# Optimization experiments

Measured on AMD Instinct MI355X. Metric: run time of the kernel, lower is better.

The kernel has to match this reference:

```python
import jax, jax.numpy as jnp
import numpy as np

N = 100_000          # nodes
E_RAND = 1_600_000   # random edges (avg degree 16)
IN, H, F, SEQ = 64, 4, 16, 10
FLAT = H * F * SEQ   # 640, MLP input width
MLP_DIMS = [FLAT, 180, 150, 128, 80, 64, 32, 1]


def setup_inputs() -> dict:
    key = jax.random.key(0)
    ks = jax.random.split(key, 32)
    x = jax.random.normal(ks[0], (N, IN), jnp.float32)
    # edges + self loops (dgl.add_self_loop)
    src = jnp.concatenate([jax.random.randint(ks[1], (E_RAND,), 0, N), jnp.arange(N)]).astype(jnp.int32)
    dst = jnp.concatenate([jax.random.randint(ks[2], (E_RAND,), 0, N), jnp.arange(N)]).astype(jnp.int32)
    inp = {"x": x, "src": src, "dst": dst}
    # GATConv params (fc has no bias in DGL; bias added post-aggregation)
    inp["fc_w"] = (jax.random.normal(ks[3], (IN, H * F), jnp.float32) / np.sqrt(IN).astype(np.float32))
    inp["bias"] = jnp.zeros((H * F,), jnp.float32)
    inp["attn_l"] = jax.random.normal(ks[4], (H, F), jnp.float32) * 0.1
    inp["attn_r"] = jax.random.normal(ks[5], (H, F), jnp.float32) * 0.1
    # deep MLP params
    for i in range(7):
        di, do = MLP_DIMS[i], MLP_DIMS[i + 1]
        inp[f"w{i+1}"] = jax.random.normal(ks[6 + i], (di, do), jnp.float32) / np.sqrt(di).astype(np.float32)
        inp[f"b{i+1}"] = jnp.zeros((do,), jnp.float32)
    inp["wt"] = jax.random.normal(ks[20], (FLAT, 1), jnp.float32) / np.sqrt(FLAT).astype(np.float32)
    return inp


def reference(x, src, dst, fc_w, bias, attn_l, attn_r,
              w1, b1, w2, b2, w3, b3, w4, b4, w5, b5, w6, b6, w7, b7, wt):
    # --- GATConv ---
    feat = (x @ fc_w).reshape(N, H, F)                      # [N,H,F]
    el = jnp.einsum('nhf,hf->nh', feat, attn_l)             # [N,H]
    er = jnp.einsum('nhf,hf->nh', feat, attn_r)
    e = jax.nn.leaky_relu(el[src] + er[dst], 0.2)           # [E,H]
    # edge softmax over incoming edges of each dst node
    m = jax.ops.segment_max(e, dst, num_segments=N)         # [N,H]
    ez = jnp.exp(e - m[dst])
    denom = jax.ops.segment_sum(ez, dst, num_segments=N)
    alpha = ez / denom[dst]                                 # [E,H]
    msg = alpha[:, :, None] * feat[src]                     # [E,H,F]
    out = jax.ops.segment_sum(msg, dst, num_segments=N) + bias.reshape(1, H, F)
    # --- flatten SEQ nodes per path, deep MLP + linear_trans ---
    g = out.reshape(N // SEQ, FLAT)                         # [P,640]
    h = g
    layers = [(w1, b1), (w2, b2), (w3, b3), (w4, b4), (w5, b5), (w6, b6), (w7, b7)]
    for i, (w, b) in enumerate(layers):
        h = h @ w + b
        if i < len(layers) - 1:
            h = jax.nn.relu(h)
    wx = g @ wt                                             # [P,1]
    return h + wx
```

## Files before the change

### kernel.cpp

```cpp
#include <hip/hip_runtime.h>
#include <hip/hip_bf16.h>
#include <hip/hip_fp16.h>

#define N_NODES 100000
#define P_PATHS 10000
#define NBUK 391
#define FEAT_BLKS 391
#define HIST_BLKS 416
#define WPREP_BLKS 94

typedef __attribute__((ext_vector_type(8))) short s16x8;
typedef __attribute__((ext_vector_type(4))) short s16x4;
typedef __attribute__((ext_vector_type(4))) float f32x4;
typedef __attribute__((ext_vector_type(8))) _Float16 f16x8;

__device__ __forceinline__ short f2bf(float v) {
    return __builtin_bit_cast(short, __float2bfloat16(v));
}
__device__ __forceinline__ float bf2f(short s) {
    return __bfloat162float(__builtin_bit_cast(__hip_bfloat16, s));
}
__device__ __forceinline__ float h2f(short s) {
    return __half2float(__builtin_bit_cast(__half, s));
}
__device__ __forceinline__ short f2h(float v) {
    return __builtin_bit_cast(short, __float2half(v));
}

__global__ __launch_bounds__(256) void k_fused1(const float* __restrict__ x,
                                                const float* __restrict__ fc_w,
                                                const float* __restrict__ attn_l,
                                                const float* __restrict__ attn_r,
                                                __half* __restrict__ feat,
                                                float* __restrict__ el,
                                                float* __restrict__ er,
                                                const int* __restrict__ dst,
                                                int* __restrict__ buktot,
                                                const float* __restrict__ w1,
                                                const float* __restrict__ w2,
                                                const float* __restrict__ w3,
                                                const float* __restrict__ w4,
                                                const float* __restrict__ w5,
                                                const float* __restrict__ w6,
                                                short* __restrict__ wf, int E) {
    __shared__ float s_w[64 * 64];
    __shared__ float s_wx[64 * 16];
    __shared__ int hcnt[NBUK];
    int tid = threadIdx.x;
    int bb = blockIdx.x;

    if (bb < FEAT_BLKS) {
        for (int i = tid; i < 4096; i += 256) s_w[i] = fc_w[i];
        __syncthreads();
        for (int i = tid; i < 1024; i += 256) {
            int k = i >> 4, c = i & 15;
            float v = 0.f;
            if (c < 8) {
                int h = c & 3;
                const float* av = (c < 4) ? attn_l : attn_r;
                for (int f = 0; f < 16; ++f) v += s_w[k * 64 + h * 16 + f] * av[h * 16 + f];
            }
            s_wx[i] = v;
        }
        __syncthreads();

        int w = tid >> 6, l = tid & 63;
        int c_lane = l & 15, kg = l >> 4;

        s16x8 wh[5][2], wlo[5][2];
#pragma unroll
        for (int ct = 0; ct < 5; ++ct)
#pragma unroll
            for (int ks = 0; ks < 2; ++ks) {
                s16x8 h8, l8;
#pragma unroll
                for (int i = 0; i < 8; ++i) {
                    int k = ks * 32 + kg * 8 + i;
                    float v = (ct < 4) ? s_w[k * 64 + ct * 16 + c_lane]
                                       : s_wx[k * 16 + c_lane];
                    short hi = f2bf(v);
                    h8[i] = hi;
                    l8[i] = f2bf(v - bf2f(hi));
                }
                wh[ct][ks] = h8;
                wlo[ct][ks] = l8;
            }

        int nbase = bb * 256 + w * 64;
#pragma unroll 1
        for (int mt = 0; mt < 4; ++mt) {
            int m0 = nbase + mt * 16;
            if (m0 >= N_NODES) break;
            int arow = m0 + c_lane;
            size_t axoff = (size_t)(arow < N_NODES ? arow : N_NODES - 1) * 64;
            s16x8 ah[2], alo[2];
#pragma unroll
            for (int ks = 0; ks < 2; ++ks) {
                const float* xp = x + axoff + ks * 32 + kg * 8;
                float4 v0 = *(const float4*)xp;
                float4 v1 = *(const float4*)(xp + 4);
                float vv[8] = {v0.x, v0.y, v0.z, v0.w, v1.x, v1.y, v1.z, v1.w};
                s16x8 h8, l8;
#pragma unroll
                for (int i = 0; i < 8; ++i) {
                    short hi = f2bf(vv[i]);
                    h8[i] = hi;
                    l8[i] = f2bf(vv[i] - bf2f(hi));
                }
                ah[ks] = h8;
                alo[ks] = l8;
            }
            int r0 = m0 + kg * 4;
#pragma unroll
            for (int ct = 0; ct < 5; ++ct) {
                f32x4 acc = {0.f, 0.f, 0.f, 0.f};
#pragma unroll
                for (int ks = 0; ks < 2; ++ks) {
                    acc = __builtin_amdgcn_mfma_f32_16x16x32_bf16(ah[ks], wh[ct][ks], acc, 0, 0, 0);
                    acc = __builtin_amdgcn_mfma_f32_16x16x32_bf16(ah[ks], wlo[ct][ks], acc, 0, 0, 0);
                    acc = __builtin_amdgcn_mfma_f32_16x16x32_bf16(alo[ks], wh[ct][ks], acc, 0, 0, 0);
                }
                if (ct < 4) {
#pragma unroll
                    for (int j = 0; j < 4; ++j) {
                        int r = r0 + j;
                        if (r < N_NODES)
                            feat[(size_t)r * 64 + ct * 16 + c_lane] = __float2half(acc[j]);
                    }
                } else {
                    if (c_lane < 4) {
#pragma unroll
                        for (int j = 0; j < 4; ++j) {
                            int r = r0 + j;
                            if (r < N_NODES) el[r * 4 + c_lane] = acc[j];
                        }
                    } else if (c_lane < 8) {
#pragma unroll
                        for (int j = 0; j < 4; ++j) {
                            int r = r0 + j;
                            if (r < N_NODES) er[r * 4 + (c_lane - 4)] = acc[j];
                        }
                    }
                }
            }
        }
    } else if (bb < FEAT_BLKS + HIST_BLKS) {
        int hb = bb - FEAT_BLKS;
        for (int i = tid; i < NBUK; i += 256) hcnt[i] = 0;
        __syncthreads();
#pragma unroll
        for (int j = 0; j < 4; ++j) {
            int i = hb * 4096 + j * 1024 + tid * 4;
            if (i + 3 < E) {
                int4 d4 = *(const int4*)(dst + i);
                atomicAdd(&hcnt[d4.x >> 8], 1);
                atomicAdd(&hcnt[d4.y >> 8], 1);
                atomicAdd(&hcnt[d4.z >> 8], 1);
                atomicAdd(&hcnt[d4.w >> 8], 1);
            } else {
                for (int k = i; k < E && k < i + 4; ++k)
                    atomicAdd(&hcnt[dst[k] >> 8], 1);
            }
        }
        __syncthreads();
        for (int i = tid; i < NBUK; i += 256)
            if (hcnt[i]) atomicAdd(buktot + i, hcnt[i]);
    } else {
        const int nblk[6] = {240, 60, 40, 20, 12, 4};
        const int din_[6] = {640, 180, 150, 128, 80, 64};
        const int dout_[6] = {180, 150, 128, 80, 64, 32};
        const int ks_[6]  = {20, 6, 5, 4, 3, 2};
        const int off_[6] = {0, 122880, 153600, 174080, 184320, 190464};
        const float* wp[6] = {w1, w2, w3, w4, w5, w6};

        int b = (bb - FEAT_BLKS - HIST_BLKS) * 4 + (tid >> 6);
        int layer = 0;
        while (layer < 5 && b >= nblk[layer]) { b -= nblk[layer]; ++layer; }
        int KS = ks_[layer];
        int ct = b / KS, ks = b % KS;
        int l = tid & 63;
        int c = ct * 16 + (l & 15);
        int k0 = ks * 32 + ((l >> 4) * 8);
        int din = din_[layer], dout = dout_[layer];
        const float* w = wp[layer];
        s16x8 vh;
#pragma unroll
        for (int i = 0; i < 8; ++i) {
            int k = k0 + i;
            float v = (k < din && c < dout) ? w[k * dout + c] : 0.f;
            vh[i] = f2h(v);
        }
        size_t o = (size_t)off_[layer] + ((size_t)(ct * KS + ks) * 64 + l) * 8;
        *(s16x8*)(wf + o) = vh;
    }
}

__global__ __launch_bounds__(512) void k_scanB(const int* __restrict__ buktot,
                                               int* __restrict__ bukstart,
                                               int* __restrict__ bukptr,
                                               int* __restrict__ rowptr, int E) {
    __shared__ int s[512];
    int tid = threadIdx.x;
    int v = (tid < NBUK) ? buktot[tid] : 0;
    s[tid] = v;
    __syncthreads();
    for (int off = 1; off < 512; off <<= 1) {
        int t = (tid >= off) ? s[tid - off] : 0;
        __syncthreads();
        s[tid] += t;
        __syncthreads();
    }
    int excl = s[tid] - v;
    if (tid < NBUK) { bukstart[tid] = excl; bukptr[tid] = excl; }
    if (tid == 0) { bukstart[NBUK] = E; rowptr[N_NODES] = E; }
}

__global__ __launch_bounds__(256) void k_bucketA(const int* __restrict__ src,
                                                 const int* __restrict__ dst,
                                                 int* __restrict__ bukptr,
                                                 unsigned* __restrict__ pair, int E) {
    __shared__ int cnt[NBUK];
    __shared__ int base[NBUK];
    int tid = threadIdx.x;
    for (int i = tid; i < NBUK; i += 256) cnt[i] = 0;
    __syncthreads();
    int b0 = blockIdx.x * 2048;
    int s[8], d[8], off[8];
#pragma unroll
    for (int j = 0; j < 8; ++j) {
        int i = b0 + j * 256 + tid;
        if (i < E) {
            s[j] = src[i];
            d[j] = dst[i];
            off[j] = atomicAdd(&cnt[d[j] >> 8], 1);
        } else {
            d[j] = -1; s[j] = 0; off[j] = 0;
        }
    }
    __syncthreads();
    for (int i = tid; i < NBUK; i += 256)
        base[i] = cnt[i] ? atomicAdd(bukptr + i, cnt[i]) : 0;
    __syncthreads();
#pragma unroll
    for (int j = 0; j < 8; ++j) {
        if (d[j] >= 0) {
            int pos = base[d[j] >> 8] + off[j];
            pair[pos] = (unsigned)s[j] | ((unsigned)(d[j] & 255) << 17);
        }
    }
}

__global__ __launch_bounds__(256) void k_bucketC(const unsigned* __restrict__ pair,
                                                 const int* __restrict__ bukstart,
                                                 int* __restrict__ rowptr,
                                                 int* __restrict__ csr, int E) {
    __shared__ int cnt[256];
    __shared__ int s[256];
    __shared__ int wofs[256];
    int buk = blockIdx.x, tid = threadIdx.x;
    int p0 = bukstart[buk], p1 = bukstart[buk + 1];
    cnt[tid] = 0;
    __syncthreads();
    for (int i = p0 + tid; i < p1; i += 256)
        atomicAdd(&cnt[pair[i] >> 17], 1);
    __syncthreads();
    int v = cnt[tid];
    s[tid] = v;
    __syncthreads();
    for (int off = 1; off < 256; off <<= 1) {
        int t = (tid >= off) ? s[tid - off] : 0;
        __syncthreads();
        s[tid] += t;
        __syncthreads();
    }
    int r = p0 + s[tid] - v;
    wofs[tid] = r;
    int node = (buk << 8) + tid;
    if (node < N_NODES) rowptr[node] = r;
    __syncthreads();
    for (int i = p0 + tid; i < p1; i += 256) {
        unsigned p = pair[i];
        int pos = atomicAdd(&wofs[p >> 17], 1);
        csr[pos] = (int)(p & 0x1FFFFu);
    }
}

__global__ __launch_bounds__(256) void k_agg(const int* __restrict__ rowptr,
                                             const int* __restrict__ csr,
                                             const float* __restrict__ el,
                                             const float* __restrict__ er,
                                             const __half* __restrict__ feat,
                                             const float* __restrict__ bias,
                                             __half* __restrict__ agg) {
    int tid = threadIdx.x;
    int wave = tid >> 6, lane = tid & 63;
    int slot = lane >> 4;
    int fl = lane & 15;
    int n = blockIdx.x * 4 + wave;
    if (n >= N_NODES) return;
    int h = fl >> 2;
    float ern = er[(size_t)n * 4 + h];
    int e0 = rowptr[n], e1 = rowptr[n + 1];
    f32x4 a0 = {0.f, 0.f, 0.f, 0.f}, a1 = {0.f, 0.f, 0.f, 0.f};
    float den0 = 0.f, den1 = 0.f;
    int e = e0 + slot;
    for (; e + 4 < e1; e += 8) {
        int s0 = csr[e], s1 = csr[e + 4];
        s16x4 v0 = *(const s16x4*)(feat + (size_t)s0 * 64 + fl * 4);
        s16x4 v1 = *(const s16x4*)(feat + (size_t)s1 * 64 + fl * 4);
        float ev0 = el[(size_t)s0 * 4 + h] + ern;
        float ev1 = el[(size_t)s1 * 4 + h] + ern;
        ev0 = ev0 > 0.f ? ev0 : 0.2f * ev0;
        ev1 = ev1 > 0.f ? ev1 : 0.2f * ev1;
        float ez0 = __expf(ev0);
        float ez1 = __expf(ev1);
#pragma unroll
        for (int t = 0; t < 4; ++t) {
            a0[t] += ez0 * h2f(v0[t]);
            a1[t] += ez1 * h2f(v1[t]);
        }
        den0 += ez0;
        den1 += ez1;
    }
    for (; e < e1; e += 4) {
        int s0 = csr[e];
        s16x4 v0 = *(const s16x4*)(feat + (size_t)s0 * 64 + fl * 4);
        float ev0 = el[(size_t)s0 * 4 + h] + ern;
        ev0 = ev0 > 0.f ? ev0 : 0.2f * ev0;
        float ez0 = __expf(ev0);
#pragma unroll
        for (int t = 0; t < 4; ++t)
            a0[t] += ez0 * h2f(v0[t]);
        den0 += ez0;
    }
    f32x4 a;
    float den = den0 + den1;
#pragma unroll
    for (int t = 0; t < 4; ++t) a[t] = a0[t] + a1[t];
#pragma unroll
    for (int t = 0; t < 4; ++t) {
        a[t] += __shfl_xor(a[t], 32);
        a[t] += __shfl_xor(a[t], 16);
    }
    den += __shfl_xor(den, 32);
    den += __shfl_xor(den, 16);
    if (slot == 0) {
        float inv = 1.f / den;
        s16x4 o;
        o[0] = f2h(a[0] * inv + bias[fl * 4 + 0]);
        o[1] = f2h(a[1] * inv + bias[fl * 4 + 1]);
        o[2] = f2h(a[2] * inv + bias[fl * 4 + 2]);
        o[3] = f2h(a[3] * inv + bias[fl * 4 + 3]);
        *(s16x4*)(agg + (size_t)n * 64 + fl * 4) = o;
    }
}

template <int KS, int CT>
__device__ __forceinline__ void mfma_layer16(const short* sa, int sstride,
                                             short* dst_,
                                             const short* __restrict__ wf,
                                             const float* __restrict__ bias,
                                             int dout, int w, int l) {
    int abase = (l & 15) * sstride + ((l >> 4) * 8);
    int c_lane = l & 15;
    for (int ct = w; ct < CT; ct += 4) {
        f32x4 acc = {0.f, 0.f, 0.f, 0.f};
        const f16x8* wp = (const f16x8*)wf + (size_t)(ct * KS) * 64 + l;
#pragma unroll
        for (int ks = 0; ks < KS; ++ks) {
            f16x8 av = *(const f16x8*)(sa + abase + ks * 32);
            f16x8 wv = wp[ks * 64];
            acc = __builtin_amdgcn_mfma_f32_16x16x32_f16(av, wv, acc, 0, 0, 0);
        }
        int c = ct * 16 + c_lane;
        float bb = (c < dout) ? bias[c] : 0.f;
        int row0 = (l >> 4) * 4;
#pragma unroll
        for (int j = 0; j < 4; ++j) {
            float v = acc[j] + bb;
            v = v > 0.f ? v : 0.f;
            dst_[(row0 + j) * 200 + c] = f2h(v);
        }
    }
}

__global__ __launch_bounds__(256) void k_mlp(const __half* __restrict__ agg,
                                             const short* __restrict__ wf,
                                             const float* __restrict__ b1,
                                             const float* __restrict__ b2,
                                             const float* __restrict__ b3,
                                             const float* __restrict__ b4,
                                             const float* __restrict__ b5,
                                             const float* __restrict__ b6,
                                             const float* __restrict__ w7,
                                             const float* __restrict__ b7,
                                             const float* __restrict__ wt,
                                             float* __restrict__ outp) {
    __shared__ __align__(16) short smem[13600];
    __shared__ float wx[16];
    short* g  = smem;
    short* h0 = smem + 10368;
    short* h1 = smem;

    int tid = threadIdx.x;
    int w = tid >> 6, l = tid & 63;
    int p0 = blockIdx.x * 16;

    const s16x8* a8 = (const s16x8*)(agg + (size_t)p0 * 640);
    for (int i = tid; i < 16 * 80; i += 256) {
        int r = i / 80, c8 = (i % 80) * 8;
        *(s16x8*)(g + r * 648 + c8) = a8[i];
    }

    if (tid < 128) {
        int path = tid >> 3, sub = tid & 7;
        const __half* gr = agg + (size_t)(p0 + path) * 640;
        float acc = 0.f;
        for (int k = sub * 4; k < 640; k += 32) {
            s16x4 gv = *(const s16x4*)(gr + k);
            float4 wv = *(const float4*)(wt + k);
            acc += h2f(gv[0]) * wv.x + h2f(gv[1]) * wv.y
                 + h2f(gv[2]) * wv.z + h2f(gv[3]) * wv.w;
        }
        acc += __shfl_xor(acc, 1);
        acc += __shfl_xor(acc, 2);
        acc += __shfl_xor(acc, 4);
        if (sub == 0) wx[path] = acc;
    }
    __syncthreads();

    mfma_layer16<20, 12>(g, 648, h0, wf + 0,      b1, 180, w, l);
    __syncthreads();
    mfma_layer16<6, 10>(h0, 200, h1, wf + 122880, b2, 150, w, l);
    __syncthreads();
    mfma_layer16<5, 8>(h1, 200, h0, wf + 153600, b3, 128, w, l);
    __syncthreads();
    mfma_layer16<4, 5>(h0, 200, h1, wf + 174080, b4, 80, w, l);
    {
        int r = tid >> 4, c = 80 + (tid & 15);
        h1[r * 200 + c] = 0;
    }
    __syncthreads();
    mfma_layer16<3, 4>(h1, 200, h0, wf + 184320, b5, 64, w, l);
    __syncthreads();
    mfma_layer16<2, 2>(h0, 200, h1, wf + 190464, b6, 32, w, l);
    __syncthreads();

    if (tid < 16) {
        float acc = b7[0];
#pragma unroll
        for (int k = 0; k < 32; ++k)
            acc += h2f(h1[tid * 200 + k]) * w7[k];
        outp[p0 + tid] = acc + wx[tid];
    }
}

extern "C" void kernel_launch(void* const* d_in, const int* in_sizes, int n_in,
                              void* d_out, int out_size, void* d_ws, size_t ws_size,
                              hipStream_t stream) {
    const float* x      = (const float*)d_in[0];
    const int*   src    = (const int*)d_in[1];
    const int*   dst    = (const int*)d_in[2];
    const float* fc_w   = (const float*)d_in[3];
    const float* bias   = (const float*)d_in[4];
    const float* attn_l = (const float*)d_in[5];
    const float* attn_r = (const float*)d_in[6];
    const float* w1 = (const float*)d_in[7];  const float* b1 = (const float*)d_in[8];
    const float* w2 = (const float*)d_in[9];  const float* b2 = (const float*)d_in[10];
    const float* w3 = (const float*)d_in[11]; const float* b3 = (const float*)d_in[12];
    const float* w4 = (const float*)d_in[13]; const float* b4 = (const float*)d_in[14];
    const float* w5 = (const float*)d_in[15]; const float* b5 = (const float*)d_in[16];
    const float* w6 = (const float*)d_in[17]; const float* b6 = (const float*)d_in[18];
    const float* w7 = (const float*)d_in[19]; const float* b7 = (const float*)d_in[20];
    const float* wt = (const float*)d_in[21];
    int E = in_sizes[1];

    float* ws      = (float*)d_ws;
    __half* feat   = (__half*)ws;
    float* el      = ws + 6400000;
    float* er      = ws + 6800000;
    __half* agg    = (__half*)(ws + 7200000);
    unsigned* pair = (unsigned*)(ws + 10400000);
    int*   rowptr  = (int*)(ws + 13600000);
    int*   buktot  = (int*)(ws + 13700004);
    int*   bukstart= (int*)(ws + 13700400);
    int*   bukptr  = (int*)(ws + 13700800);
    int*   csr     = (int*)(ws + 13701200);
    short* wf      = (short*)(ws + 13701200 + E);

    int nwgA = (E + 2047) / 2048;

    hipMemsetAsync(buktot, 0, NBUK * 4, stream);

    k_fused1<<<FEAT_BLKS + HIST_BLKS + WPREP_BLKS, 256, 0, stream>>>(
        x, fc_w, attn_l, attn_r, feat, el, er, dst, buktot,
        w1, w2, w3, w4, w5, w6, wf, E);
    k_scanB<<<1, 512, 0, stream>>>(buktot, bukstart, bukptr, rowptr, E);
    k_bucketA<<<nwgA, 256, 0, stream>>>(src, dst, bukptr, pair, E);
    k_bucketC<<<NBUK, 256, 0, stream>>>(pair, bukstart, rowptr, csr, E);
    k_agg<<<N_NODES / 4, 256, 0, stream>>>(rowptr, csr, el, er, feat, bias, agg);
    k_mlp<<<P_PATHS / 16, 256, 0, stream>>>(agg, wf, b1, b2, b3, b4, b5, b6,
                                            w7, b7, wt, (float*)d_out);
}
```

Baseline: 168.3 us.

## Widen aggregation gathers to 16-byte loads and split feature GEMM across more blocks

The aggregation kernel now gives each lane 8 half features (a 16-byte load) instead of 4, so 8 lanes cover a node's row and 8 edges are in flight per wave instead of 4. This should raise memory-level parallelism for the random gathers and cut per-edge index and exp work per feature. The cost is one extra shuffle stage in the reduction and more accumulator registers. Separately, the feature-projection kernel processes half as many rows per block with twice as many blocks, trading repeated per-block weight splitting for more parallelism.

```diff
diff --git a/kernel.cpp b/kernel.cpp
--- a/kernel.cpp
+++ b/kernel.cpp
@@ -5,7 +5,7 @@
 #define N_NODES 100000
 #define P_PATHS 10000
 #define NBUK 391
-#define FEAT_BLKS 391
+#define FEAT_BLKS 782
 #define HIST_BLKS 416
 #define WPREP_BLKS 94
 
@@ -86,9 +86,9 @@
                 wlo[ct][ks] = l8;
             }
 
-        int nbase = bb * 256 + w * 64;
+        int nbase = bb * 128 + w * 32;
 #pragma unroll 1
-        for (int mt = 0; mt < 4; ++mt) {
+        for (int mt = 0; mt < 2; ++mt) {
             int m0 = nbase + mt * 16;
             if (m0 >= N_NODES) break;
             int arow = m0 + c_lane;
@@ -294,20 +294,21 @@
                                              __half* __restrict__ agg) {
     int tid = threadIdx.x;
     int wave = tid >> 6, lane = tid & 63;
-    int slot = lane >> 4;
-    int fl = lane & 15;
+    int slot = lane >> 3;
+    int fl = lane & 7;
     int n = blockIdx.x * 4 + wave;
     if (n >= N_NODES) return;
-    int h = fl >> 2;
+    int h = fl >> 1;
     float ern = er[(size_t)n * 4 + h];
     int e0 = rowptr[n], e1 = rowptr[n + 1];
-    f32x4 a0 = {0.f, 0.f, 0.f, 0.f}, a1 = {0.f, 0.f, 0.f, 0.f};
+    f32x4 a0 = {0.f,0.f,0.f,0.f}, b0 = {0.f,0.f,0.f,0.f};
+    f32x4 a1 = {0.f,0.f,0.f,0.f}, b1 = {0.f,0.f,0.f,0.f};
     float den0 = 0.f, den1 = 0.f;
     int e = e0 + slot;
-    for (; e + 4 < e1; e += 8) {
-        int s0 = csr[e], s1 = csr[e + 4];
-        s16x4 v0 = *(const s16x4*)(feat + (size_t)s0 * 64 + fl * 4);
-        s16x4 v1 = *(const s16x4*)(feat + (size_t)s1 * 64 + fl * 4);
+    for (; e + 8 < e1; e += 16) {
+        int s0 = csr[e], s1 = csr[e + 8];
+        s16x8 v0 = *(const s16x8*)(feat + (size_t)s0 * 64 + fl * 8);
+        s16x8 v1 = *(const s16x8*)(feat + (size_t)s1 * 64 + fl * 8);
         float ev0 = el[(size_t)s0 * 4 + h] + ern;
         float ev1 = el[(size_t)s1 * 4 + h] + ern;
         ev0 = ev0 > 0.f ? ev0 : 0.2f * ev0;
@@ -317,41 +318,51 @@
 #pragma unroll
         for (int t = 0; t < 4; ++t) {
             a0[t] += ez0 * h2f(v0[t]);
+            b0[t] += ez0 * h2f(v0[t + 4]);
             a1[t] += ez1 * h2f(v1[t]);
+            b1[t] += ez1 * h2f(v1[t + 4]);
         }
         den0 += ez0;
         den1 += ez1;
     }
-    for (; e < e1; e += 4) {
+    for (; e < e1; e += 8) {
         int s0 = csr[e];
-        s16x4 v0 = *(const s16x4*)(feat + (size_t)s0 * 64 + fl * 4);
+        s16x8 v0 = *(const s16x8*)(feat + (size_t)s0 * 64 + fl * 8);
         float ev0 = el[(size_t)s0 * 4 + h] + ern;
         ev0 = ev0 > 0.f ? ev0 : 0.2f * ev0;
         float ez0 = __expf(ev0);
 #pragma unroll
-        for (int t = 0; t < 4; ++t)
+        for (int t = 0; t < 4; ++t) {
             a0[t] += ez0 * h2f(v0[t]);
+            b0[t] += ez0 * h2f(v0[t + 4]);
+        }
         den0 += ez0;
     }
-    f32x4 a;
     float den = den0 + den1;
-#pragma unroll
-    for (int t = 0; t < 4; ++t) a[t] = a0[t] + a1[t];
+    f32x4 a, b;
+#pragma unroll
+    for (int t = 0; t < 4; ++t) { a[t] = a0[t] + a1[t]; b[t] = b0[t] + b1[t]; }
 #pragma unroll
     for (int t = 0; t < 4; ++t) {
         a[t] += __shfl_xor(a[t], 32);
         a[t] += __shfl_xor(a[t], 16);
+        a[t] += __shfl_xor(a[t], 8);
+        b[t] += __shfl_xor(b[t], 32);
+        b[t] += __shfl_xor(b[t], 16);
+        b[t] += __shfl_xor(b[t], 8);
     }
     den += __shfl_xor(den, 32);
     den += __shfl_xor(den, 16);
+    den += __shfl_xor(den, 8);
     if (slot == 0) {
         float inv = 1.f / den;
-        s16x4 o;
-        o[0] = f2h(a[0] * inv + bias[fl * 4 + 0]);
-        o[1] = f2h(a[1] * inv + bias[fl * 4 + 1]);
-        o[2] = f2h(a[2] * inv + bias[fl * 4 + 2]);
-        o[3] = f2h(a[3] * inv + bias[fl * 4 + 3]);
-        *(s16x4*)(agg + (size_t)n * 64 + fl * 4) = o;
+        s16x8 o;
+#pragma unroll
+        for (int t = 0; t < 4; ++t) {
+            o[t]     = f2h(a[t] * inv + bias[fl * 8 + t]);
+            o[t + 4] = f2h(b[t] * inv + bias[fl * 8 + t + 4]);
+        }
+        *(s16x8*)(agg + (size_t)n * 64 + fl * 8) = o;
     }
 }
 
```

New measurement: 159.1 us. 1.06x faster.
